# Optimization experiments

Measured on AMD Instinct MI355X. Metric: run time of the kernel, lower is better.

The kernel has to match this reference:

```python
import jax, jax.numpy as jnp
import numpy as np

N_NODES = 20000
N_EDGES = 200000
C = 64             # channel multiplicity (hidden_irreps = 64x0e + 64x1o)
LMAX = 3
NLM = (LMAX + 1) ** 2   # 16 spherical-harmonic components
NUM_ELEM = 10
R_DIM = 8          # radial embedding out dim
MLP_H = 64
AVG_NEI = 10.0
L_OF_LM = np.repeat(np.arange(LMAX + 1), 2 * np.arange(LMAX + 1) + 1)  # [16] l index per lm slot


def setup_inputs() -> dict:
    key = jax.random.key(0)
    k = jax.random.split(key, 16)
    f32 = jnp.float32
    elems = jax.random.randint(k[0], (N_NODES,), 0, NUM_ELEM)
    one_hot = jax.nn.one_hot(elems, NUM_ELEM, dtype=f32)
    node_features = jax.random.normal(k[1], (N_NODES, C), dtype=f32)
    angular_embedding = jax.random.normal(k[2], (N_EDGES, NLM), dtype=f32)
    radial_embedding = jax.random.normal(k[3], (N_EDGES, R_DIM), dtype=f32)
    edge_index = jax.random.randint(k[4], (2, N_EDGES), 0, N_NODES)

    def w(kk, shape, fan_in):  # e3nn-style 1/sqrt(fan_in) normalization baked into init
        return jax.random.normal(kk, shape, dtype=f32) / float(np.sqrt(fan_in))

    W_up = w(k[5], (C, C), C)
    W_mlp1 = w(k[6], (R_DIM, MLP_H), R_DIM)
    W_mlp2 = w(k[7], (MLP_H, MLP_H), MLP_H)
    W_mlp3 = w(k[8], (MLP_H, MLP_H), MLP_H)
    W_mlp4 = w(k[9], (MLP_H, (LMAX + 1) * C), MLP_H)
    W_lin = w(k[10], (LMAX + 1, C, C), C)
    W_skip = w(k[11], (C, NUM_ELEM, C), C * NUM_ELEM)
    W_c0 = jax.random.normal(k[12], (NUM_ELEM, C), dtype=f32)
    W_c1 = jax.random.normal(k[13], (NUM_ELEM, C), dtype=f32)
    W_p0 = w(k[14], (C, C), C)
    W_p1 = w(k[15], (C, C), C)
    return dict(node_features=node_features, one_hot=one_hot,
                angular_embedding=angular_embedding, radial_embedding=radial_embedding,
                W_up=W_up, W_mlp1=W_mlp1, W_mlp2=W_mlp2, W_mlp3=W_mlp3, W_mlp4=W_mlp4,
                W_lin=W_lin, W_skip=W_skip, W_c0=W_c0, W_c1=W_c1, W_p0=W_p0, W_p1=W_p1,
                edge_index=edge_index)


def reference(node_features, one_hot, angular_embedding, radial_embedding,
              W_up, W_mlp1, W_mlp2, W_mlp3, W_mlp4, W_lin, W_skip,
              W_c0, W_c1, W_p0, W_p1, edge_index):
    sender, receiver = edge_index[0], edge_index[1]
    n = node_features.shape[0]
    # ---- interaction block (RealAgnosticResidual; node feats are pure scalars 64x0e) ----
    x = node_features @ W_up                                    # linear_up [N,C]
    h = jax.nn.silu(radial_embedding @ W_mlp1)                  # radial MLP -> per-edge TP weights
    h = jax.nn.silu(h @ W_mlp2)
    h = jax.nn.silu(h @ W_mlp3)
    tp_w = (h @ W_mlp4).reshape(-1, LMAX + 1, C)                # [E,4,C] (one weight per l path, uvu)
    w_lm = tp_w[:, L_OF_LM, :]                                  # [E,16,C]
    # uvu tensor product of 0e node feats with spherical harmonics (CG trivial for 0e x l -> l)
    msg = x[sender][:, None, :] * angular_embedding[:, :, None] * w_lm   # [E,16,C]
    agg = jax.ops.segment_sum(msg, receiver, num_segments=n) / AVG_NEI   # scatter-sum [N,16,C]
    feats = jnp.einsum('nmc,mck->nmk', agg, W_lin[L_OF_LM])     # per-l channel-mixing linear [N,16,C]
    # residual skip FCTP(64x0e, 10x0e -> hidden): only the 0e block is connected
    sc0 = jnp.einsum('nc,na,cak->nk', node_features, one_hot, W_skip)    # [N,C]
    # ---- equivariant product basis block (correlation = 1) ----
    wn0 = one_hot @ W_c0                                        # element-dependent weights [N,C]
    wn1 = one_hot @ W_c1
    f0 = feats[:, 0, :] * wn0                                   # l=0 output [N,C]
    f1 = feats[:, 1:4, :] * wn1[:, None, :]                     # l=1 output [N,3,C]
    out0 = f0 @ W_p0 + sc0                                      # [N,C]
    out1 = jnp.einsum('nmc,ck->nmk', f1, W_p1)                  # [N,3,C] (sc 1o block is zero)
    # flatten to e3nn channel-major irreps layout -> node_env [N, C*(1+3)]
    return jnp.concatenate([out0, jnp.swapaxes(out1, 1, 2).reshape(n, -1)], axis=-1)
```

## Files before the change

### kernel.cpp

```cpp
#include <hip/hip_runtime.h>

typedef __attribute__((ext_vector_type(8))) short s16x8;
typedef __attribute__((ext_vector_type(4))) float f32x4;

__device__ inline float bf2f(ushort u) {
    union { unsigned int i; float f; } v; v.i = ((unsigned)u) << 16; return v.f;
}
__device__ inline float u2f(unsigned u) {
    union { unsigned int i; float f; } v; v.i = u; return v.f;
}
__device__ inline ushort f2bf(float f) {
    union { float f; unsigned int i; } v; v.f = f;
    unsigned r = v.i + 0x7FFFu + ((v.i >> 16) & 1u);
    return (ushort)(r >> 16);
}
__device__ inline unsigned cvt_pk(float lo, float hi) {
    unsigned d;
    asm("v_cvt_pk_bf16_f32 %0, %1, %2" : "=v"(d) : "v"(lo), "v"(hi));
    return d;
}
__device__ inline float silu_f(float x) {
    float e;
    asm("v_exp_f32 %0, %1" : "=v"(e) : "v"(x * -1.44269504f));
    float d = 1.f + e, r;
    asm("v_rcp_f32 %0, %1" : "=v"(r) : "v"(d));
    return x * r;
}

__global__ __launch_bounds__(256) void prep_up_kernel(
    const float* __restrict__ nf, const float* __restrict__ W_up,
    ushort* __restrict__ x_ws,
    const float* __restrict__ W1, const float* __restrict__ W2,
    const float* __restrict__ W3, const float* __restrict__ W4,
    const float* __restrict__ W_lin, const float* __restrict__ Wp0,
    const float* __restrict__ Wp1, const float* __restrict__ W_skip,
    ushort* __restrict__ wimg, int* __restrict__ counts, int N) {
    __shared__ float sW[64 * 64];
    __shared__ float sNf[32][64];
    int tid = threadIdx.x;
    int nub = N / 32;
    if ((int)blockIdx.x < nub) {
        size_t n0 = (size_t)blockIdx.x * 32;
        for (int i = tid; i < 4096; i += 256) sW[i] = W_up[i];
        for (int i = tid; i < 2048; i += 256) {
            int r = i >> 6, c = i & 63;
            sNf[r][c] = nf[(n0 + r) * 64 + c];
        }
        __syncthreads();
        int r = tid >> 3, k0 = (tid & 7) * 8;
        float acc[8] = {0, 0, 0, 0, 0, 0, 0, 0};
        #pragma unroll 4
        for (int c = 0; c < 64; ++c) {
            float v = sNf[r][c];
            const float* wr = &sW[c * 64 + k0];
            #pragma unroll
            for (int j = 0; j < 8; ++j) acc[j] += v * wr[j];
        }
        uint4 val;
        val.x = cvt_pk(acc[0], acc[1]);
        val.y = cvt_pk(acc[2], acc[3]);
        val.z = cvt_pk(acc[4], acc[5]);
        val.w = cvt_pk(acc[6], acc[7]);
        *(uint4*)(x_ws + (n0 + r) * 64 + k0) = val;
        return;
    }
    int idx = ((int)blockIdx.x - nub) * 256 + tid;
    if (idx < N) counts[idx] = 0;
    if (idx < 4096) {
        int m = idx >> 6, k = idx & 63;
        int dst = m * 64 + ((((k >> 3) ^ (m & 7))) << 3) + (k & 7);
        wimg[dst] = (k < 8) ? f2bf(W1[k * 64 + m]) : (ushort)0;
    } else if (idx < 8192) {
        int i = idx - 4096;
        int m = i >> 6, k = i & 63;
        int dst = 4096 + m * 64 + ((((k >> 3) ^ (m & 7))) << 3) + (k & 7);
        wimg[dst] = f2bf(W2[k * 64 + m]);
    } else if (idx < 12288) {
        int i = idx - 8192;
        int m = i >> 6, k = i & 63;
        int dst = 8192 + m * 64 + ((((k >> 3) ^ (m & 7))) << 3) + (k & 7);
        wimg[dst] = f2bf(W3[k * 64 + m]);
    } else if (idx < 20480) {
        int i = idx - 12288;
        int m = i >> 6, k = i & 63;
        int dst = 12288 + m * 64 + ((((k >> 3) ^ (m & 7))) << 3) + (k & 7);
        wimg[dst] = f2bf(W4[k * 256 + m]);
    } else if (idx < 29696) {
        int i = idx - 20480;
        int row = i / 72, k = i % 72;
        int l = row >> 6, col = row & 63;
        wimg[idx] = (k < 64) ? f2bf(W_lin[l * 4096 + k * 64 + col]) : (ushort)0;
    } else if (idx < 38912) {
        int i = idx - 29696;
        int row = i / 72, k = i % 72;
        int l = row >> 6, col = row & 63;
        const float* Wp = l ? Wp1 : Wp0;
        wimg[idx] = (k < 64) ? f2bf(Wp[k * 64 + col]) : (ushort)0;
    } else if (idx < 79872) {
        int i = idx - 38912;
        wimg[idx] = f2bf(W_skip[i]);
    }
}

__global__ __launch_bounds__(256) void hist_kernel(const int* __restrict__ recv,
                                                   int* __restrict__ counts, int E) {
    int e = blockIdx.x * 256 + threadIdx.x;
    if (e < E) atomicAdd(&counts[recv[e]], 1);
}

__global__ __launch_bounds__(1024) void scan_kernel(const int* __restrict__ counts,
                                                    int* __restrict__ offsets,
                                                    int* __restrict__ cursor, int n) {
    __shared__ int wsums[16];
    int tid = threadIdx.x, lane = tid & 63, wid = tid >> 6;
    int CH = (n + 1023) >> 10;
    int base = tid * CH;
    int cnt[20];
    int tot = 0;
    if (CH <= 20) {
        #pragma unroll
        for (int j = 0; j < 20; ++j) {
            int i = base + j;
            cnt[j] = (j < CH && i < n) ? counts[i] : 0;
            tot += cnt[j];
        }
    } else {
        for (int j = 0; j < CH; ++j) {
            int i = base + j;
            if (i < n) tot += counts[i];
        }
    }
    int v = tot;
    for (int off = 1; off < 64; off <<= 1) {
        int t = __shfl_up(v, off, 64);
        if (lane >= off) v += t;
    }
    if (lane == 63) wsums[wid] = v;
    __syncthreads();
    if (tid == 0) {
        int acc = 0;
        for (int w = 0; w < 16; ++w) { int t = wsums[w]; wsums[w] = acc; acc += t; }
    }
    __syncthreads();
    int excl = wsums[wid] + v - tot;
    if (CH <= 20) {
        #pragma unroll
        for (int j = 0; j < 20; ++j) {
            int i = base + j;
            if (j < CH && i < n) {
                offsets[i] = excl; cursor[i] = excl; excl += cnt[j];
            }
        }
    } else {
        for (int j = 0; j < CH; ++j) {
            int i = base + j;
            if (i < n) { offsets[i] = excl; cursor[i] = excl; excl += counts[i]; }
        }
    }
    if (tid == 1023) offsets[n] = excl;
}

__global__ __launch_bounds__(256) void edge_mlp_kernel(
    const int* __restrict__ recv, const float* __restrict__ radial,
    int* __restrict__ cursor, int* __restrict__ csr_eid,
    const ushort* __restrict__ wimg, unsigned* __restrict__ tpw32, int E) {
    __shared__ __align__(16) ushort sW4[8192];
    __shared__ __align__(16) ushort sB[4][1024];
    int tid = threadIdx.x, lane = tid & 63, wave = tid >> 6;
    int n = lane & 15, hi = lane >> 4;

    for (int i = tid; i < 1024; i += 256)
        ((s16x8*)sW4)[i] = ((const s16x8*)(wimg + 12288))[i];

    s16x8 w1f[4], w2f[4][2], w3f[4][2];
    #pragma unroll
    for (int mt = 0; mt < 4; ++mt) {
        int row = mt * 16 + n, r7 = row & 7;
        w1f[mt] = *(const s16x8*)(wimg + row * 64 + ((hi ^ r7) << 3));
        #pragma unroll
        for (int ks = 0; ks < 2; ++ks) {
            w2f[mt][ks] = *(const s16x8*)(wimg + 4096 + row * 64 + (((ks * 4 + hi) ^ r7) << 3));
            w3f[mt][ks] = *(const s16x8*)(wimg + 8192 + row * 64 + (((ks * 4 + hi) ^ r7) << 3));
        }
    }
    __syncthreads();

    char* myB = (char*)sB[wave];
    int n7 = n & 7;

    for (int sub = 0; sub < 2; ++sub) {
        int base = blockIdx.x * 128 + wave * 32 + sub * 16;
        if (base >= E) break;
        int e = base + n;
        bool oke = e < E;
        int eC = min(e, E - 1);

        s16x8 bR;
        #pragma unroll
        for (int j = 0; j < 8; ++j) bR[j] = 0;
        if (hi == 0) {
            float4 r0 = *(const float4*)(radial + (size_t)eC * 8);
            float4 r1 = *(const float4*)(radial + (size_t)eC * 8 + 4);
            union { s16x8 v; uint4 u; } bb;
            bb.u.x = cvt_pk(r0.x, r0.y);
            bb.u.y = cvt_pk(r0.z, r0.w);
            bb.u.z = cvt_pk(r1.x, r1.y);
            bb.u.w = cvt_pk(r1.z, r1.w);
            bR = bb.v;
            if (oke) {
                int pos = atomicAdd(&cursor[recv[e]], 1);
                csr_eid[pos] = e;
            }
        }

        f32x4 zero = {0.f, 0.f, 0.f, 0.f};
        f32x4 d[4];
        #pragma unroll
        for (int mt = 0; mt < 4; ++mt)
            d[mt] = __builtin_amdgcn_mfma_f32_16x16x32_bf16(w1f[mt], bR, zero, 0, 0, 0);

        #pragma unroll
        for (int mt = 0; mt < 4; ++mt) {
            uint2 val = {cvt_pk(silu_f(d[mt][0]), silu_f(d[mt][1])),
                         cvt_pk(silu_f(d[mt][2]), silu_f(d[mt][3]))};
            int slot = mt * 2 + (hi >> 1);
            *(uint2*)(myB + n * 128 + ((slot ^ n7) << 4) + (hi & 1) * 8) = val;
        }
        s16x8 b0 = *(const s16x8*)(myB + n * 128 + ((hi ^ n7) << 4));
        s16x8 b1 = *(const s16x8*)(myB + n * 128 + (((4 + hi) ^ n7) << 4));

        #pragma unroll
        for (int mt = 0; mt < 4; ++mt) {
            d[mt] = __builtin_amdgcn_mfma_f32_16x16x32_bf16(w2f[mt][0], b0, zero, 0, 0, 0);
            d[mt] = __builtin_amdgcn_mfma_f32_16x16x32_bf16(w2f[mt][1], b1, d[mt], 0, 0, 0);
        }
        #pragma unroll
        for (int mt = 0; mt < 4; ++mt) {
            uint2 val = {cvt_pk(silu_f(d[mt][0]), silu_f(d[mt][1])),
                         cvt_pk(silu_f(d[mt][2]), silu_f(d[mt][3]))};
            int slot = mt * 2 + (hi >> 1);
            *(uint2*)(myB + n * 128 + ((slot ^ n7) << 4) + (hi & 1) * 8) = val;
        }
        b0 = *(const s16x8*)(myB + n * 128 + ((hi ^ n7) << 4));
        b1 = *(const s16x8*)(myB + n * 128 + (((4 + hi) ^ n7) << 4));

        #pragma unroll
        for (int mt = 0; mt < 4; ++mt) {
            d[mt] = __builtin_amdgcn_mfma_f32_16x16x32_bf16(w3f[mt][0], b0, zero, 0, 0, 0);
            d[mt] = __builtin_amdgcn_mfma_f32_16x16x32_bf16(w3f[mt][1], b1, d[mt], 0, 0, 0);
        }
        #pragma unroll
        for (int mt = 0; mt < 4; ++mt) {
            uint2 val = {cvt_pk(silu_f(d[mt][0]), silu_f(d[mt][1])),
                         cvt_pk(silu_f(d[mt][2]), silu_f(d[mt][3]))};
            int slot = mt * 2 + (hi >> 1);
            *(uint2*)(myB + n * 128 + ((slot ^ n7) << 4) + (hi & 1) * 8) = val;
        }
        b0 = *(const s16x8*)(myB + n * 128 + ((hi ^ n7) << 4));
        b1 = *(const s16x8*)(myB + n * 128 + (((4 + hi) ^ n7) << 4));

        size_t rowbase = (size_t)e * 64;
        #pragma unroll
        for (int mt = 0; mt < 4; ++mt) {
            int row0 = mt * 16 + n, r70 = row0 & 7;
            int row1 = (mt + 4) * 16 + n, r71 = row1 & 7;
            s16x8 a0lo = *(const s16x8*)(sW4 + row0 * 64 + ((hi ^ r70) << 3));
            s16x8 a1lo = *(const s16x8*)(sW4 + row0 * 64 + (((4 + hi) ^ r70) << 3));
            s16x8 a0hi = *(const s16x8*)(sW4 + row1 * 64 + ((hi ^ r71) << 3));
            s16x8 a1hi = *(const s16x8*)(sW4 + row1 * 64 + (((4 + hi) ^ r71) << 3));
            f32x4 olo = __builtin_amdgcn_mfma_f32_16x16x32_bf16(a0lo, b0, zero, 0, 0, 0);
            olo = __builtin_amdgcn_mfma_f32_16x16x32_bf16(a1lo, b1, olo, 0, 0, 0);
            f32x4 ohi = __builtin_amdgcn_mfma_f32_16x16x32_bf16(a0hi, b0, zero, 0, 0, 0);
            ohi = __builtin_amdgcn_mfma_f32_16x16x32_bf16(a1hi, b1, ohi, 0, 0, 0);
            if (oke) {
                uint4 val;
                val.x = cvt_pk(olo[0], ohi[0]);
                val.y = cvt_pk(olo[1], ohi[1]);
                val.z = cvt_pk(olo[2], ohi[2]);
                val.w = cvt_pk(olo[3], ohi[3]);
                *(uint4*)(tpw32 + rowbase + mt * 16 + hi * 4) = val;
            }
        }
    }
}

__global__ __launch_bounds__(256) void agg_kernel(const float* __restrict__ angular,
                                                  const int* __restrict__ sender,
                                                  const int* __restrict__ csr_eid,
                                                  const unsigned* __restrict__ tpw32,
                                                  const int* __restrict__ offsets,
                                                  const ushort* __restrict__ x_ws,
                                                  ushort* __restrict__ agg, int N) {
    int wave = threadIdx.x >> 6, lane = threadIdx.x & 63;
    int node = blockIdx.x * 4 + wave;
    if (node >= N) return;
    int beg = offsets[node], end = offsets[node + 1];
    float a0 = 0, a1 = 0, a2 = 0, a3 = 0;
    for (int cb = beg; cb < end; cb += 64) {
        int m = min(64, end - cb);
        int ev = csr_eid[cb + min(lane, m - 1)];
        int sv = sender[ev];
        for (int e0 = 0; e0 < m; e0 += 4) {
            unsigned t[4];
            ushort x[4];
            float4 g[4];
            #pragma unroll
            for (int j = 0; j < 4; ++j) {
                int e = e0 + j;
                int ec = min(e, m - 1);
                int eidj = __shfl(ev, ec);
                t[j] = tpw32[(size_t)eidj * 64 + lane];
                x[j] = x_ws[(size_t)__shfl(sv, ec) * 64 + lane];
                if (e < m) g[j] = *(const float4*)(angular + (size_t)eidj * 16);
                else g[j] = make_float4(0.f, 0.f, 0.f, 0.f);
            }
            #pragma unroll
            for (int j = 0; j < 4; ++j) {
                float xv = bf2f(x[j]);
                float tp0 = u2f(t[j] << 16);
                float tp1 = u2f(t[j] & 0xffff0000u);
                float y0 = xv * tp0, y1 = xv * tp1;
                a0 += g[j].x * y0;
                a1 += g[j].y * y1;
                a2 += g[j].z * y1;
                a3 += g[j].w * y1;
            }
        }
    }
    size_t b = (size_t)node * 256 + lane;
    agg[b] = f2bf(a0 * 0.1f);
    agg[b + 64] = f2bf(a1 * 0.1f);
    agg[b + 128] = f2bf(a2 * 0.1f);
    agg[b + 192] = f2bf(a3 * 0.1f);
}

__global__ __launch_bounds__(256) void node_out2_kernel(
    const float* __restrict__ nf, const float* __restrict__ one_hot,
    const ushort* __restrict__ wimg, const float* __restrict__ W_c0,
    const float* __restrict__ W_c1, const ushort* __restrict__ agg,
    float* __restrict__ out) {
    __shared__ __align__(16) ushort sWl[2 * 64 * 72];
    __shared__ __align__(16) ushort sF[4][32 * 72];
    __shared__ float sSc[32][64];
    __shared__ float sWc[2][640];
    __shared__ int sElem[32];
    int tid = threadIdx.x;
    int n0 = blockIdx.x * 32;
    int lane = tid & 63, m = tid >> 6;
    int lsel = (m == 0) ? 0 : 1;

    s16x8 pf[4][2];
    #pragma unroll
    for (int nt = 0; nt < 4; ++nt)
        #pragma unroll
        for (int ks = 0; ks < 2; ++ks)
            pf[nt][ks] = *(const s16x8*)(wimg + 29696 +
                (lsel * 64 + nt * 16 + (lane & 15)) * 72 + ks * 32 + (lane >> 4) * 8);

    for (int i = tid; i < 1152; i += 256)
        ((s16x8*)sWl)[i] = ((const s16x8*)(wimg + 20480))[i];
    for (int i = tid; i < 1280; i += 256)
        sWc[i >= 640][i % 640] = (i >= 640 ? W_c1 : W_c0)[i % 640];
    if (tid < 32) {
        int nn = n0 + tid, e = 0;
        for (int a = 0; a < 10; ++a)
            if (one_hot[(size_t)nn * 10 + a] > 0.5f) { e = a; break; }
        sElem[tid] = e;
    }
    __syncthreads();

    {
        int nl = tid >> 3, k0 = (tid & 7) * 8;
        int nn = n0 + nl, elem = sElem[nl];
        float acc[8] = {0, 0, 0, 0, 0, 0, 0, 0};
        const ushort* wskb = wimg + 38912;
        for (int c = 0; c < 64; ++c) {
            float v = nf[(size_t)nn * 64 + c];
            s16x8 w = *(const s16x8*)(wskb + ((size_t)c * 10 + elem) * 64 + k0);
            #pragma unroll
            for (int j = 0; j < 8; ++j) acc[j] += v * bf2f((ushort)w[j]);
        }
        #pragma unroll
        for (int j = 0; j < 8; ++j) sSc[nl][k0 + j] = acc[j];
    }

    f32x4 acc[2][4] = {};
    s16x8 afr[2][2];
    #pragma unroll
    for (int mt = 0; mt < 2; ++mt)
        #pragma unroll
        for (int ks = 0; ks < 2; ++ks)
            afr[mt][ks] = *(const s16x8*)(agg +
                (((size_t)(n0 + mt * 16 + (lane & 15))) * 4 + m) * 64 +
                ks * 32 + (lane >> 4) * 8);
    #pragma unroll
    for (int nt = 0; nt < 4; ++nt)
        #pragma unroll
        for (int ks = 0; ks < 2; ++ks) {
            s16x8 b = *(const s16x8*)(sWl + (lsel * 64 + nt * 16 + (lane & 15)) * 72 +
                                      ks * 32 + (lane >> 4) * 8);
            #pragma unroll
            for (int mt = 0; mt < 2; ++mt)
                acc[mt][nt] = __builtin_amdgcn_mfma_f32_16x16x32_bf16(afr[mt][ks], b,
                                                                      acc[mt][nt], 0, 0, 0);
        }

    #pragma unroll
    for (int mt = 0; mt < 2; ++mt)
        #pragma unroll
        for (int nt = 0; nt < 4; ++nt)
            #pragma unroll
            for (int r = 0; r < 4; ++r) {
                int nl = mt * 16 + (lane >> 4) * 4 + r;
                int k = nt * 16 + (lane & 15);
                float scale = sWc[lsel][sElem[nl] * 64 + k];
                sF[m][nl * 72 + k] = f2bf(acc[mt][nt][r] * scale);
            }
    __syncthreads();

    f32x4 acc2[2][4] = {};
    s16x8 af2[2][2];
    #pragma unroll
    for (int mt = 0; mt < 2; ++mt)
        #pragma unroll
        for (int ks = 0; ks < 2; ++ks)
            af2[mt][ks] = *(const s16x8*)(&sF[m][(mt * 16 + (lane & 15)) * 72 +
                                                 ks * 32 + (lane >> 4) * 8]);
    #pragma unroll
    for (int nt = 0; nt < 4; ++nt)
        #pragma unroll
        for (int ks = 0; ks < 2; ++ks) {
            #pragma unroll
            for (int mt = 0; mt < 2; ++mt)
                acc2[mt][nt] = __builtin_amdgcn_mfma_f32_16x16x32_bf16(af2[mt][ks],
                                                                       pf[nt][ks],
                                                                       acc2[mt][nt], 0, 0, 0);
        }

    #pragma unroll
    for (int mt = 0; mt < 2; ++mt)
        #pragma unroll
        for (int nt = 0; nt < 4; ++nt)
            #pragma unroll
            for (int r = 0; r < 4; ++r) {
                int nl = mt * 16 + (lane >> 4) * 4 + r;
                int k = nt * 16 + (lane & 15);
                size_t nn = (size_t)n0 + nl;
                if (m == 0)
                    out[nn * 256 + k] = acc2[mt][nt][r] + sSc[nl][k];
                else
                    out[nn * 256 + 64 + k * 3 + (m - 1)] = acc2[mt][nt][r];
            }
}

extern "C" void kernel_launch(void* const* d_in, const int* in_sizes, int n_in,
                              void* d_out, int out_size, void* d_ws, size_t ws_size,
                              hipStream_t stream) {
    const float* node_features = (const float*)d_in[0];
    const float* one_hot = (const float*)d_in[1];
    const float* angular = (const float*)d_in[2];
    const float* radial = (const float*)d_in[3];
    const float* W_up = (const float*)d_in[4];
    const float* W_mlp1 = (const float*)d_in[5];
    const float* W_mlp2 = (const float*)d_in[6];
    const float* W_mlp3 = (const float*)d_in[7];
    const float* W_mlp4 = (const float*)d_in[8];
    const float* W_lin = (const float*)d_in[9];
    const float* W_skip = (const float*)d_in[10];
    const float* W_c0 = (const float*)d_in[11];
    const float* W_c1 = (const float*)d_in[12];
    const float* W_p0 = (const float*)d_in[13];
    const float* W_p1 = (const float*)d_in[14];
    const int* edge_index = (const int*)d_in[15];
    float* out = (float*)d_out;

    int N = in_sizes[0] / 64;
    int E = in_sizes[2] / 16;
    const int* sender = edge_index;
    const int* receiver = edge_index + E;

    char* p = (char*)d_ws;
    ushort* x_ws = (ushort*)p;      p += (size_t)N * 64 * 2;
    unsigned* tpw32 = (unsigned*)p; p += (size_t)E * 64 * 4;
    ushort* agg = (ushort*)p;       p += (size_t)N * 256 * 2;
    ushort* wimg = (ushort*)p;      p += 79872 * 2;
    int* counts = (int*)p;          p += (size_t)N * 4;
    int* offsets = (int*)p;         p += (size_t)(N + 1) * 4;
    int* cursor = (int*)p;          p += (size_t)N * 4;
    int* csr_eid = (int*)p;         p += (size_t)E * 4;

    prep_up_kernel<<<N / 32 + 312, 256, 0, stream>>>(node_features, W_up, x_ws,
                                                     W_mlp1, W_mlp2, W_mlp3, W_mlp4,
                                                     W_lin, W_p0, W_p1, W_skip, wimg,
                                                     counts, N);
    hist_kernel<<<(E + 255) / 256, 256, 0, stream>>>(receiver, counts, E);
    scan_kernel<<<1, 1024, 0, stream>>>(counts, offsets, cursor, N);
    edge_mlp_kernel<<<(E + 127) / 128, 256, 0, stream>>>(receiver, radial, cursor,
                                                         csr_eid, wimg, tpw32, E);
    agg_kernel<<<(N + 3) / 4, 256, 0, stream>>>(angular, sender, csr_eid, tpw32,
                                                offsets, x_ws, agg, N);
    node_out2_kernel<<<N / 32, 256, 0, stream>>>(node_features, one_hot, wimg,
                                                 W_c0, W_c1, agg, out);
}
```

Before: 120.0 us.

## Record edge ranks in histogram and interleave two edge tiles in edge MLP

The histogram kernel now stores each edge's atomic rank within its receiver, so the edge MLP places edges into the CSR with offset+rank instead of a second atomic on a cursor array. The edge MLP drops the shared-memory staging of W4 and the register-cached weights, loading weight fragments straight from global/L2 per layer. It processes both 16-edge sub-tiles together so each weight fragment feeds two MFMAs, giving more independent work per wave. This removes a block-wide barrier and the shared-memory weight copy, at the cost of repeated global weight loads per wave and an extra rank array write and read.

```diff
diff --git a/kernel.cpp b/kernel.cpp
--- a/kernel.cpp
+++ b/kernel.cpp
@@ -103,14 +103,14 @@
 }
 
 __global__ __launch_bounds__(256) void hist_kernel(const int* __restrict__ recv,
-                                                   int* __restrict__ counts, int E) {
+                                                   int* __restrict__ counts,
+                                                   int* __restrict__ rank, int E) {
     int e = blockIdx.x * 256 + threadIdx.x;
-    if (e < E) atomicAdd(&counts[recv[e]], 1);
+    if (e < E) rank[e] = atomicAdd(&counts[recv[e]], 1);
 }
 
 __global__ __launch_bounds__(1024) void scan_kernel(const int* __restrict__ counts,
-                                                    int* __restrict__ offsets,
-                                                    int* __restrict__ cursor, int n) {
+                                                    int* __restrict__ offsets, int n) {
     __shared__ int wsums[16];
     int tid = threadIdx.x, lane = tid & 63, wid = tid >> 6;
     int CH = (n + 1023) >> 10;
@@ -147,139 +147,164 @@
         #pragma unroll
         for (int j = 0; j < 20; ++j) {
             int i = base + j;
-            if (j < CH && i < n) {
-                offsets[i] = excl; cursor[i] = excl; excl += cnt[j];
-            }
+            if (j < CH && i < n) { offsets[i] = excl; excl += cnt[j]; }
         }
     } else {
         for (int j = 0; j < CH; ++j) {
             int i = base + j;
-            if (i < n) { offsets[i] = excl; cursor[i] = excl; excl += counts[i]; }
+            if (i < n) { offsets[i] = excl; excl += counts[i]; }
         }
     }
     if (tid == 1023) offsets[n] = excl;
 }
 
 __global__ __launch_bounds__(256) void edge_mlp_kernel(
-    const int* __restrict__ recv, const float* __restrict__ radial,
-    int* __restrict__ cursor, int* __restrict__ csr_eid,
-    const ushort* __restrict__ wimg, unsigned* __restrict__ tpw32, int E) {
-    __shared__ __align__(16) ushort sW4[8192];
-    __shared__ __align__(16) ushort sB[4][1024];
+    const int* __restrict__ recv, const int* __restrict__ rank,
+    const int* __restrict__ offsets, const float* __restrict__ radial,
+    int* __restrict__ csr_eid, const ushort* __restrict__ wimg,
+    unsigned* __restrict__ tpw32, int E) {
+    __shared__ __align__(16) ushort sB[4][2048];
     int tid = threadIdx.x, lane = tid & 63, wave = tid >> 6;
     int n = lane & 15, hi = lane >> 4;
-
-    for (int i = tid; i < 1024; i += 256)
-        ((s16x8*)sW4)[i] = ((const s16x8*)(wimg + 12288))[i];
-
-    s16x8 w1f[4], w2f[4][2], w3f[4][2];
+    int base = blockIdx.x * 128 + wave * 32;
+    if (base >= E) return;
+    int eA = base + n, eB = base + 16 + n;
+    bool okA = eA < E, okB = eB < E;
+    int eAc = min(eA, E - 1), eBc = min(eB, E - 1);
+
+    char* bAq = (char*)sB[wave];
+    char* bBq = (char*)sB[wave] + 2048;
+    int n7 = n & 7;
+
+    s16x8 bRA, bRB;
+    #pragma unroll
+    for (int j = 0; j < 8; ++j) { bRA[j] = 0; bRB[j] = 0; }
+    if (hi == 0) {
+        float4 a0 = *(const float4*)(radial + (size_t)eAc * 8);
+        float4 a1 = *(const float4*)(radial + (size_t)eAc * 8 + 4);
+        float4 c0 = *(const float4*)(radial + (size_t)eBc * 8);
+        float4 c1 = *(const float4*)(radial + (size_t)eBc * 8 + 4);
+        union { s16x8 v; uint4 u; } pa, pb;
+        pa.u.x = cvt_pk(a0.x, a0.y); pa.u.y = cvt_pk(a0.z, a0.w);
+        pa.u.z = cvt_pk(a1.x, a1.y); pa.u.w = cvt_pk(a1.z, a1.w);
+        pb.u.x = cvt_pk(c0.x, c0.y); pb.u.y = cvt_pk(c0.z, c0.w);
+        pb.u.z = cvt_pk(c1.x, c1.y); pb.u.w = cvt_pk(c1.z, c1.w);
+        bRA = pa.v; bRB = pb.v;
+        if (okA) csr_eid[offsets[recv[eA]] + rank[eA]] = eA;
+        if (okB) csr_eid[offsets[recv[eB]] + rank[eB]] = eB;
+    }
+
+    f32x4 zero = {0.f, 0.f, 0.f, 0.f};
+    f32x4 dA[4], dB[4];
+
     #pragma unroll
     for (int mt = 0; mt < 4; ++mt) {
         int row = mt * 16 + n, r7 = row & 7;
-        w1f[mt] = *(const s16x8*)(wimg + row * 64 + ((hi ^ r7) << 3));
-        #pragma unroll
-        for (int ks = 0; ks < 2; ++ks) {
-            w2f[mt][ks] = *(const s16x8*)(wimg + 4096 + row * 64 + (((ks * 4 + hi) ^ r7) << 3));
-            w3f[mt][ks] = *(const s16x8*)(wimg + 8192 + row * 64 + (((ks * 4 + hi) ^ r7) << 3));
-        }
-    }
-    __syncthreads();
-
-    char* myB = (char*)sB[wave];
-    int n7 = n & 7;
-
-    for (int sub = 0; sub < 2; ++sub) {
-        int base = blockIdx.x * 128 + wave * 32 + sub * 16;
-        if (base >= E) break;
-        int e = base + n;
-        bool oke = e < E;
-        int eC = min(e, E - 1);
-
-        s16x8 bR;
-        #pragma unroll
-        for (int j = 0; j < 8; ++j) bR[j] = 0;
-        if (hi == 0) {
-            float4 r0 = *(const float4*)(radial + (size_t)eC * 8);
-            float4 r1 = *(const float4*)(radial + (size_t)eC * 8 + 4);
-            union { s16x8 v; uint4 u; } bb;
-            bb.u.x = cvt_pk(r0.x, r0.y);
-            bb.u.y = cvt_pk(r0.z, r0.w);
-            bb.u.z = cvt_pk(r1.x, r1.y);
-            bb.u.w = cvt_pk(r1.z, r1.w);
-            bR = bb.v;
-            if (oke) {
-                int pos = atomicAdd(&cursor[recv[e]], 1);
-                csr_eid[pos] = e;
-            }
-        }
-
-        f32x4 zero = {0.f, 0.f, 0.f, 0.f};
-        f32x4 d[4];
-        #pragma unroll
-        for (int mt = 0; mt < 4; ++mt)
-            d[mt] = __builtin_amdgcn_mfma_f32_16x16x32_bf16(w1f[mt], bR, zero, 0, 0, 0);
-
-        #pragma unroll
-        for (int mt = 0; mt < 4; ++mt) {
-            uint2 val = {cvt_pk(silu_f(d[mt][0]), silu_f(d[mt][1])),
-                         cvt_pk(silu_f(d[mt][2]), silu_f(d[mt][3]))};
-            int slot = mt * 2 + (hi >> 1);
-            *(uint2*)(myB + n * 128 + ((slot ^ n7) << 4) + (hi & 1) * 8) = val;
-        }
-        s16x8 b0 = *(const s16x8*)(myB + n * 128 + ((hi ^ n7) << 4));
-        s16x8 b1 = *(const s16x8*)(myB + n * 128 + (((4 + hi) ^ n7) << 4));
-
-        #pragma unroll
-        for (int mt = 0; mt < 4; ++mt) {
-            d[mt] = __builtin_amdgcn_mfma_f32_16x16x32_bf16(w2f[mt][0], b0, zero, 0, 0, 0);
-            d[mt] = __builtin_amdgcn_mfma_f32_16x16x32_bf16(w2f[mt][1], b1, d[mt], 0, 0, 0);
-        }
-        #pragma unroll
-        for (int mt = 0; mt < 4; ++mt) {
-            uint2 val = {cvt_pk(silu_f(d[mt][0]), silu_f(d[mt][1])),
-                         cvt_pk(silu_f(d[mt][2]), silu_f(d[mt][3]))};
-            int slot = mt * 2 + (hi >> 1);
-            *(uint2*)(myB + n * 128 + ((slot ^ n7) << 4) + (hi & 1) * 8) = val;
-        }
-        b0 = *(const s16x8*)(myB + n * 128 + ((hi ^ n7) << 4));
-        b1 = *(const s16x8*)(myB + n * 128 + (((4 + hi) ^ n7) << 4));
-
-        #pragma unroll
-        for (int mt = 0; mt < 4; ++mt) {
-            d[mt] = __builtin_amdgcn_mfma_f32_16x16x32_bf16(w3f[mt][0], b0, zero, 0, 0, 0);
-            d[mt] = __builtin_amdgcn_mfma_f32_16x16x32_bf16(w3f[mt][1], b1, d[mt], 0, 0, 0);
-        }
-        #pragma unroll
-        for (int mt = 0; mt < 4; ++mt) {
-            uint2 val = {cvt_pk(silu_f(d[mt][0]), silu_f(d[mt][1])),
-                         cvt_pk(silu_f(d[mt][2]), silu_f(d[mt][3]))};
-            int slot = mt * 2 + (hi >> 1);
-            *(uint2*)(myB + n * 128 + ((slot ^ n7) << 4) + (hi & 1) * 8) = val;
-        }
-        b0 = *(const s16x8*)(myB + n * 128 + ((hi ^ n7) << 4));
-        b1 = *(const s16x8*)(myB + n * 128 + (((4 + hi) ^ n7) << 4));
-
-        size_t rowbase = (size_t)e * 64;
-        #pragma unroll
-        for (int mt = 0; mt < 4; ++mt) {
-            int row0 = mt * 16 + n, r70 = row0 & 7;
-            int row1 = (mt + 4) * 16 + n, r71 = row1 & 7;
-            s16x8 a0lo = *(const s16x8*)(sW4 + row0 * 64 + ((hi ^ r70) << 3));
-            s16x8 a1lo = *(const s16x8*)(sW4 + row0 * 64 + (((4 + hi) ^ r70) << 3));
-            s16x8 a0hi = *(const s16x8*)(sW4 + row1 * 64 + ((hi ^ r71) << 3));
-            s16x8 a1hi = *(const s16x8*)(sW4 + row1 * 64 + (((4 + hi) ^ r71) << 3));
-            f32x4 olo = __builtin_amdgcn_mfma_f32_16x16x32_bf16(a0lo, b0, zero, 0, 0, 0);
-            olo = __builtin_amdgcn_mfma_f32_16x16x32_bf16(a1lo, b1, olo, 0, 0, 0);
-            f32x4 ohi = __builtin_amdgcn_mfma_f32_16x16x32_bf16(a0hi, b0, zero, 0, 0, 0);
-            ohi = __builtin_amdgcn_mfma_f32_16x16x32_bf16(a1hi, b1, ohi, 0, 0, 0);
-            if (oke) {
-                uint4 val;
-                val.x = cvt_pk(olo[0], ohi[0]);
-                val.y = cvt_pk(olo[1], ohi[1]);
-                val.z = cvt_pk(olo[2], ohi[2]);
-                val.w = cvt_pk(olo[3], ohi[3]);
-                *(uint4*)(tpw32 + rowbase + mt * 16 + hi * 4) = val;
-            }
+        s16x8 w = *(const s16x8*)(wimg + row * 64 + ((hi ^ r7) << 3));
+        dA[mt] = __builtin_amdgcn_mfma_f32_16x16x32_bf16(w, bRA, zero, 0, 0, 0);
+        dB[mt] = __builtin_amdgcn_mfma_f32_16x16x32_bf16(w, bRB, zero, 0, 0, 0);
+    }
+    #pragma unroll
+    for (int mt = 0; mt < 4; ++mt) {
+        int slot = mt * 2 + (hi >> 1);
+        int off = ((slot ^ n7) << 4) + (hi & 1) * 8;
+        uint2 vA = {cvt_pk(silu_f(dA[mt][0]), silu_f(dA[mt][1])),
+                    cvt_pk(silu_f(dA[mt][2]), silu_f(dA[mt][3]))};
+        *(uint2*)(bAq + n * 128 + off) = vA;
+        uint2 vB = {cvt_pk(silu_f(dB[mt][0]), silu_f(dB[mt][1])),
+                    cvt_pk(silu_f(dB[mt][2]), silu_f(dB[mt][3]))};
+        *(uint2*)(bBq + n * 128 + off) = vB;
+    }
+    s16x8 b0A = *(const s16x8*)(bAq + n * 128 + ((hi ^ n7) << 4));
+    s16x8 b1A = *(const s16x8*)(bAq + n * 128 + (((4 + hi) ^ n7) << 4));
+    s16x8 b0B = *(const s16x8*)(bBq + n * 128 + ((hi ^ n7) << 4));
+    s16x8 b1B = *(const s16x8*)(bBq + n * 128 + (((4 + hi) ^ n7) << 4));
+
+    #pragma unroll
+    for (int mt = 0; mt < 4; ++mt) {
+        int row = mt * 16 + n, r7 = row & 7;
+        s16x8 w0 = *(const s16x8*)(wimg + 4096 + row * 64 + ((hi ^ r7) << 3));
+        s16x8 w1 = *(const s16x8*)(wimg + 4096 + row * 64 + (((4 + hi) ^ r7) << 3));
+        dA[mt] = __builtin_amdgcn_mfma_f32_16x16x32_bf16(w0, b0A, zero, 0, 0, 0);
+        dA[mt] = __builtin_amdgcn_mfma_f32_16x16x32_bf16(w1, b1A, dA[mt], 0, 0, 0);
+        dB[mt] = __builtin_amdgcn_mfma_f32_16x16x32_bf16(w0, b0B, zero, 0, 0, 0);
+        dB[mt] = __builtin_amdgcn_mfma_f32_16x16x32_bf16(w1, b1B, dB[mt], 0, 0, 0);
+    }
+    #pragma unroll
+    for (int mt = 0; mt < 4; ++mt) {
+        int slot = mt * 2 + (hi >> 1);
+        int off = ((slot ^ n7) << 4) + (hi & 1) * 8;
+        uint2 vA = {cvt_pk(silu_f(dA[mt][0]), silu_f(dA[mt][1])),
+                    cvt_pk(silu_f(dA[mt][2]), silu_f(dA[mt][3]))};
+        *(uint2*)(bAq + n * 128 + off) = vA;
+        uint2 vB = {cvt_pk(silu_f(dB[mt][0]), silu_f(dB[mt][1])),
+                    cvt_pk(silu_f(dB[mt][2]), silu_f(dB[mt][3]))};
+        *(uint2*)(bBq + n * 128 + off) = vB;
+    }
+    b0A = *(const s16x8*)(bAq + n * 128 + ((hi ^ n7) << 4));
+    b1A = *(const s16x8*)(bAq + n * 128 + (((4 + hi) ^ n7) << 4));
+    b0B = *(const s16x8*)(bBq + n * 128 + ((hi ^ n7) << 4));
+    b1B = *(const s16x8*)(bBq + n * 128 + (((4 + hi) ^ n7) << 4));
+
+    #pragma unroll
+    for (int mt = 0; mt < 4; ++mt) {
+        int row = mt * 16 + n, r7 = row & 7;
+        s16x8 w0 = *(const s16x8*)(wimg + 8192 + row * 64 + ((hi ^ r7) << 3));
+        s16x8 w1 = *(const s16x8*)(wimg + 8192 + row * 64 + (((4 + hi) ^ r7) << 3));
+        dA[mt] = __builtin_amdgcn_mfma_f32_16x16x32_bf16(w0, b0A, zero, 0, 0, 0);
+        dA[mt] = __builtin_amdgcn_mfma_f32_16x16x32_bf16(w1, b1A, dA[mt], 0, 0, 0);
+        dB[mt] = __builtin_amdgcn_mfma_f32_16x16x32_bf16(w0, b0B, zero, 0, 0, 0);
+        dB[mt] = __builtin_amdgcn_mfma_f32_16x16x32_bf16(w1, b1B, dB[mt], 0, 0, 0);
+    }
+    #pragma unroll
+    for (int mt = 0; mt < 4; ++mt) {
+        int slot = mt * 2 + (hi >> 1);
+        int off = ((slot ^ n7) << 4) + (hi & 1) * 8;
+        uint2 vA = {cvt_pk(silu_f(dA[mt][0]), silu_f(dA[mt][1])),
+                    cvt_pk(silu_f(dA[mt][2]), silu_f(dA[mt][3]))};
+        *(uint2*)(bAq + n * 128 + off) = vA;
+        uint2 vB = {cvt_pk(silu_f(dB[mt][0]), silu_f(dB[mt][1])),
+                    cvt_pk(silu_f(dB[mt][2]), silu_f(dB[mt][3]))};
+        *(uint2*)(bBq + n * 128 + off) = vB;
+    }
+    b0A = *(const s16x8*)(bAq + n * 128 + ((hi ^ n7) << 4));
+    b1A = *(const s16x8*)(bAq + n * 128 + (((4 + hi) ^ n7) << 4));
+    b0B = *(const s16x8*)(bBq + n * 128 + ((hi ^ n7) << 4));
+    b1B = *(const s16x8*)(bBq + n * 128 + (((4 + hi) ^ n7) << 4));
+
+    size_t rbA = (size_t)eA * 64, rbB = (size_t)eB * 64;
+    const ushort* w4 = wimg + 12288;
+    #pragma unroll
+    for (int mt = 0; mt < 4; ++mt) {
+        int row0 = mt * 16 + n, r70 = row0 & 7;
+        int row1 = (mt + 4) * 16 + n, r71 = row1 & 7;
+        s16x8 a0lo = *(const s16x8*)(w4 + row0 * 64 + ((hi ^ r70) << 3));
+        s16x8 a1lo = *(const s16x8*)(w4 + row0 * 64 + (((4 + hi) ^ r70) << 3));
+        s16x8 a0hi = *(const s16x8*)(w4 + row1 * 64 + ((hi ^ r71) << 3));
+        s16x8 a1hi = *(const s16x8*)(w4 + row1 * 64 + (((4 + hi) ^ r71) << 3));
+        f32x4 oloA = __builtin_amdgcn_mfma_f32_16x16x32_bf16(a0lo, b0A, zero, 0, 0, 0);
+        oloA = __builtin_amdgcn_mfma_f32_16x16x32_bf16(a1lo, b1A, oloA, 0, 0, 0);
+        f32x4 ohiA = __builtin_amdgcn_mfma_f32_16x16x32_bf16(a0hi, b0A, zero, 0, 0, 0);
+        ohiA = __builtin_amdgcn_mfma_f32_16x16x32_bf16(a1hi, b1A, ohiA, 0, 0, 0);
+        f32x4 oloB = __builtin_amdgcn_mfma_f32_16x16x32_bf16(a0lo, b0B, zero, 0, 0, 0);
+        oloB = __builtin_amdgcn_mfma_f32_16x16x32_bf16(a1lo, b1B, oloB, 0, 0, 0);
+        f32x4 ohiB = __builtin_amdgcn_mfma_f32_16x16x32_bf16(a0hi, b0B, zero, 0, 0, 0);
+        ohiB = __builtin_amdgcn_mfma_f32_16x16x32_bf16(a1hi, b1B, ohiB, 0, 0, 0);
+        if (okA) {
+            uint4 val;
+            val.x = cvt_pk(oloA[0], ohiA[0]);
+            val.y = cvt_pk(oloA[1], ohiA[1]);
+            val.z = cvt_pk(oloA[2], ohiA[2]);
+            val.w = cvt_pk(oloA[3], ohiA[3]);
+            *(uint4*)(tpw32 + rbA + mt * 16 + hi * 4) = val;
+        }
+        if (okB) {
+            uint4 val;
+            val.x = cvt_pk(oloB[0], ohiB[0]);
+            val.y = cvt_pk(oloB[1], ohiB[1]);
+            val.z = cvt_pk(oloB[2], ohiB[2]);
+            val.w = cvt_pk(oloB[3], ohiB[3]);
+            *(uint4*)(tpw32 + rbB + mt * 16 + hi * 4) = val;
         }
     }
 }
@@ -486,17 +511,18 @@
     ushort* wimg = (ushort*)p;      p += 79872 * 2;
     int* counts = (int*)p;          p += (size_t)N * 4;
     int* offsets = (int*)p;         p += (size_t)(N + 1) * 4;
-    int* cursor = (int*)p;          p += (size_t)N * 4;
+    int* rank = (int*)p;            p += (size_t)E * 4;
     int* csr_eid = (int*)p;         p += (size_t)E * 4;
 
     prep_up_kernel<<<N / 32 + 312, 256, 0, stream>>>(node_features, W_up, x_ws,
                                                      W_mlp1, W_mlp2, W_mlp3, W_mlp4,
                                                      W_lin, W_p0, W_p1, W_skip, wimg,
                                                      counts, N);
-    hist_kernel<<<(E + 255) / 256, 256, 0, stream>>>(receiver, counts, E);
-    scan_kernel<<<1, 1024, 0, stream>>>(counts, offsets, cursor, N);
-    edge_mlp_kernel<<<(E + 127) / 128, 256, 0, stream>>>(receiver, radial, cursor,
-                                                         csr_eid, wimg, tpw32, E);
+    hist_kernel<<<(E + 255) / 256, 256, 0, stream>>>(receiver, counts, rank, E);
+    scan_kernel<<<1, 1024, 0, stream>>>(counts, offsets, N);
+    edge_mlp_kernel<<<(E + 127) / 128, 256, 0, stream>>>(receiver, rank, offsets,
+                                                         radial, csr_eid, wimg,
+                                                         tpw32, E);
     agg_kernel<<<(N + 3) / 4, 256, 0, stream>>>(angular, sender, csr_eid, tpw32,
                                                 offsets, x_ws, agg, N);
     node_out2_kernel<<<N / 32, 256, 0, stream>>>(node_features, one_hot, wimg,
```

After: 107.9 us. -10.0%, faster.
